# Optimization experiments

Hardware: AMD Instinct MI355X
Metric: run time of the kernel (lower is better)

The kernel has to match this reference:

```python
import jax, jax.numpy as jnp
import numpy as np

IN_DIM, OUT_DIM = 512, 512
GRID, K, NUM_STDS = 16, 2, 4
DEGREE = 3  # hardcoded in original __call__ (bspline called with 3)
NUM_CTRL = GRID + K - 1  # 17
BATCH = 4096


def bspline_basis(t, g, degree):
    """Cox-de Boor B-spline basis.
    t: (in_dim, batch) evaluation points, g: (K,) uniform knots.
    Returns basis of shape (K-1-degree, in_dim, batch)."""
    # degree-0 indicator: g[i] <= t < g[i+1]
    B = ((g[:-1, None, None] <= t[None]) & (t[None] < g[1:, None, None])).astype(t.dtype)
    for p in range(1, degree + 1):
        left = (t[None] - g[:-(p + 1), None, None]) / (g[p:-1] - g[:-(p + 1)])[:, None, None]
        right = (g[p + 1:, None, None] - t[None]) / (g[p + 1:] - g[1:-p])[:, None, None]
        B = left * B[:-1] + right * B[1:]
    return B


def setup_inputs() -> dict:
    key = jax.random.key(0)
    k1, k2, k3 = jax.random.split(key, 3)
    limit = float(np.sqrt(6.0 / (IN_DIM + OUT_DIM)))
    x = jax.random.normal(k1, (BATCH, IN_DIM), dtype=jnp.float32)
    w_b = jnp.ones((IN_DIM, OUT_DIM), dtype=jnp.float32)
    w_s = jax.random.uniform(k2, (IN_DIM, OUT_DIM), minval=-limit, maxval=limit, dtype=jnp.float32)
    control_points = jax.random.uniform(k3, (IN_DIM, OUT_DIM, NUM_CTRL), minval=-limit, maxval=limit, dtype=jnp.float32)
    grid_width = GRID / NUM_STDS
    num_aug = GRID + 1 + 2 * K
    grid_points = jnp.linspace(-K * grid_width, GRID + K * grid_width, num_aug).astype(jnp.float32)
    bound = jnp.float32(NUM_STDS * 1.0)
    return {"x": x, "w_b": w_b, "w_s": w_s, "control_points": control_points,
            "grid_points": grid_points, "bound": bound}


def reference(x, w_b, w_s, control_points, grid_points, bound):
    bound = jax.lax.stop_gradient(bound)
    g = jax.lax.stop_gradient(grid_points)
    xt = jnp.clip(x.T, -bound, bound)                      # (in_dim, batch)
    silu = xt * jax.nn.sigmoid(xt)
    bias = jnp.einsum('io,ib->ob', w_b, silu)              # (out_dim, batch)
    basis = bspline_basis(xt, g, DEGREE)                    # (nc, in_dim, batch)
    D = w_s[:, :, None] * control_points                    # (in_dim, out_dim, nc)
    spline = jnp.einsum('ioc,cib->ob', D, basis)            # single GEMM, (out_dim, batch)
    return (bias + spline).T                                # (batch, out_dim)
```

## Files before the change

### kernel.cpp

```cpp
#include <hip/hip_runtime.h>
#include <hip/hip_bf16.h>

#define IN_DIM 512
#define OUT_DIM 512
#define BATCH 4096
#define NC 9
#define KDIM (IN_DIM * NC)
#define NCTRL 17
#define TM 128
#define TN 64
#define BK 64
#define NT (KDIM / BK)
#define BUF_ELEMS 12288
#define BUF_BYTES 24576

typedef unsigned short ushort_t;
typedef __attribute__((ext_vector_type(8))) short short8;
typedef __attribute__((ext_vector_type(4))) float f32x4;

__device__ inline ushort_t to_bf16(float f) {
    union { float f; unsigned int i; } v; v.f = f;
    unsigned int r = v.i + 0x7FFF + ((v.i >> 16) & 1);
    return (ushort_t)(r >> 16);
}

__device__ inline void gld16(const ushort_t* g, void* l) {
    __builtin_amdgcn_global_load_lds(
        (const __attribute__((address_space(1))) void*)g,
        (__attribute__((address_space(3))) void*)l, 16, 0, 0);
}


__global__ void prep_A(const float* __restrict__ w_b, const float* __restrict__ w_s,
                       const float* __restrict__ ctrl, ushort_t* __restrict__ A) {
    int tid = blockIdx.x * 256 + threadIdx.x;
    int i = tid & (IN_DIM - 1);
    int o = tid >> 9;
    float ws = w_s[i * OUT_DIM + o];
    float wb = w_b[i * OUT_DIM + o];
    const float* cp = ctrl + (size_t)(i * OUT_DIM + o) * NCTRL;
    size_t rbase = (size_t)o * KDIM;
    int swz = (o & 7) << 3;
    int k0 = i * NC;
#pragma unroll
    for (int c = 0; c < 8; c++) A[rbase + ((k0 + c) ^ swz)] = to_bf16(ws * cp[c]);
    A[rbase + ((k0 + 8) ^ swz)] = to_bf16(wb);
}

__global__ __launch_bounds__(512) void prep_B(const float* __restrict__ x,
                                              const float* __restrict__ g,
                                              const float* __restrict__ bound_p,
                                              ushort_t* __restrict__ Bt) {
    __shared__ ushort_t rowbuf[KDIM];
    int b = blockIdx.x;
    int i = threadIdx.x;
    float bound = bound_p[0];
    float t = x[(size_t)b * IN_DIM + i];
    t = fminf(fmaxf(t, -bound), bound);
    float u = (t + 8.0f) * 0.625f;
    int j = (int)u;
    j = min(max(j, 2), 7);
    float gj[6];
#pragma unroll
    for (int r = 0; r < 6; r++) gj[r] = g[j - 2 + r];
    const float invph[4] = {0.f, 0.625f, 0.3125f, 0.2083333333f};
    float Nv[4]; Nv[0] = 1.0f;
    float lv[4], rv[4];
#pragma unroll
    for (int p = 1; p <= 3; p++) {
        lv[p] = t - gj[3 - p];
        rv[p] = gj[2 + p] - t;
        float saved = 0.0f;
#pragma unroll
        for (int r = 0; r < p; r++) {
            float temp = Nv[r] * invph[p];
            Nv[r] = saved + rv[r + 1] * temp;
            saved = lv[p - r] * temp;
        }
        Nv[p] = saved;
    }
    int c0 = j - 3;
    int swz = (b & 7) << 3;
    int k0 = i * NC;
#pragma unroll
    for (int c = 0; c < 8; c++) {
        float v = 0.0f;
        v = (c == c0    ) ? Nv[0] : v;
        v = (c == c0 + 1) ? Nv[1] : v;
        v = (c == c0 + 2) ? Nv[2] : v;
        v = (c == c0 + 3) ? Nv[3] : v;
        rowbuf[(k0 + c) ^ swz] = to_bf16(v);
    }
    float sg = 1.0f / (1.0f + __expf(-t));
    rowbuf[(k0 + 8) ^ swz] = to_bf16(t * sg);
    __syncthreads();
    const uint4* s = (const uint4*)rowbuf;
    uint4* d = (uint4*)(Bt + (size_t)b * KDIM);
    d[i] = s[i];
    if (i < 64) d[512 + i] = s[512 + i];
}

__global__ __launch_bounds__(512) void gemm_kan(const ushort_t* __restrict__ A,
                                                const ushort_t* __restrict__ Bt,
                                                float* __restrict__ out) {
    __shared__ ushort_t ring[4 * BUF_ELEMS];
    int tid = threadIdx.x;
    int lane = tid & 63;
    int w = tid >> 6;
    int bid = blockIdx.x;
    int ot = bid >> 5;
    int bt = bid & 31;
    int brow0 = bt * TM;
    int ocol0 = ot * TN;

    int wr = w >> 1;
    int wc = w & 1;

    f32x4 acc[2][2];
#pragma unroll
    for (int m = 0; m < 2; m++)
#pragma unroll
        for (int n = 0; n < 2; n++) acc[m][n] = (f32x4){0.f, 0.f, 0.f, 0.f};

    int lr = lane >> 3;
    int lcb = (lane & 7) * 8;
    const ushort_t* src[3];
    int ldsoff[3];
#pragma unroll
    for (int i = 0; i < 3; i++) {
        int f = w * 3 + i;
        const ushort_t* basep = (f < 16)
            ? Bt + (size_t)(brow0 + f * 8 + lr) * KDIM
            : A  + (size_t)(ocol0 + (f - 16) * 8 + lr) * KDIM;
        src[i] = basep + lcb;
        ldsoff[i] = f * 1024;
    }
    char* ringb = (char*)ring;

#define STAGE(T) do { int bb_ = ((T) & 3) * BUF_BYTES;                         \
    _Pragma("unroll") for (int i_ = 0; i_ < 3; i_++)                           \
        gld16(src[i_] + (size_t)(T) * BK, ringb + bb_ + ldsoff[i_]); } while (0)

#define COMPUTE(T) do {                                                        \
    const ushort_t* Xs_ = ring + ((T) & 3) * BUF_ELEMS;                        \
    const ushort_t* Ys_ = Xs_ + TM * BK;                                       \
    int xrow_ = wr * 32 + (lane & 15);                                         \
    int yrow_ = wc * 32 + (lane & 15);                                         \
    int swz_ = (lane & 7) << 3;                                                \
    _Pragma("unroll") for (int kk_ = 0; kk_ < 2; kk_++) {                      \
        int kofs_ = (kk_ * 32 + ((lane >> 4) << 3)) ^ swz_;                    \
        short8 xf0 = *(const short8*)&Xs_[(xrow_     ) * BK + kofs_];          \
        short8 xf1 = *(const short8*)&Xs_[(xrow_ + 16) * BK + kofs_];          \
        short8 yf0 = *(const short8*)&Ys_[(yrow_     ) * BK + kofs_];          \
        short8 yf1 = *(const short8*)&Ys_[(yrow_ + 16) * BK + kofs_];          \
        acc[0][0] = __builtin_amdgcn_mfma_f32_16x16x32_bf16(xf0, yf0, acc[0][0], 0, 0, 0); \
        acc[0][1] = __builtin_amdgcn_mfma_f32_16x16x32_bf16(xf0, yf1, acc[0][1], 0, 0, 0); \
        acc[1][0] = __builtin_amdgcn_mfma_f32_16x16x32_bf16(xf1, yf0, acc[1][0], 0, 0, 0); \
        acc[1][1] = __builtin_amdgcn_mfma_f32_16x16x32_bf16(xf1, yf1, acc[1][1], 0, 0, 0); \
    } } while (0)

#define WAITVM(N) asm volatile("s_waitcnt vmcnt(" #N ")" ::: "memory")
#define BARRIER() do { __builtin_amdgcn_sched_barrier(0);                      \
    __builtin_amdgcn_s_barrier();                                             \
    __builtin_amdgcn_sched_barrier(0);                                        \
    asm volatile("" ::: "memory"); } while (0)

    STAGE(0); STAGE(1); STAGE(2);
    for (int t = 0; t < NT - 3; ++t) {
        WAITVM(6);
        BARRIER();
        STAGE(t + 3);
        COMPUTE(t);
    }
    WAITVM(6); BARRIER(); COMPUTE(NT - 3);
    WAITVM(3); BARRIER(); COMPUTE(NT - 2);
    WAITVM(0); BARRIER(); COMPUTE(NT - 1);

    int rgrp = (lane >> 4) * 4;
    int cidx = lane & 15;
#pragma unroll
    for (int m = 0; m < 2; m++) {
#pragma unroll
        for (int n = 0; n < 2; n++) {
            int o_idx = ocol0 + wc * 32 + n * 16 + cidx;
            int b_base = brow0 + wr * 32 + m * 16 + rgrp;
#pragma unroll
            for (int r = 0; r < 4; r++)
                out[(size_t)(b_base + r) * OUT_DIM + o_idx] = acc[m][n][r];
        }
    }
#undef STAGE
#undef COMPUTE
#undef WAITVM
#undef BARRIER
}

extern "C" void kernel_launch(void* const* d_in, const int* in_sizes, int n_in,
                              void* d_out, int out_size, void* d_ws, size_t ws_size,
                              hipStream_t stream) {
    const float* x     = (const float*)d_in[0];
    const float* w_b   = (const float*)d_in[1];
    const float* w_s   = (const float*)d_in[2];
    const float* ctrl  = (const float*)d_in[3];
    const float* g     = (const float*)d_in[4];
    const float* bound = (const float*)d_in[5];
    float* out = (float*)d_out;

    ushort_t* Abuf = (ushort_t*)d_ws;
    ushort_t* Bbuf = (ushort_t*)((char*)d_ws + (size_t)(8u << 20));

    prep_A<<<IN_DIM * OUT_DIM / 256, 256, 0, stream>>>(w_b, w_s, ctrl, Abuf);
    prep_B<<<BATCH, 512, 0, stream>>>(x, g, bound, Bbuf);
    gemm_kan<<<(BATCH / TM) * (OUT_DIM / TN), 512, 0, stream>>>(Abuf, Bbuf, out);
}
```

Baseline: 52.44 us.

## Enlarge GEMM tile to 128x128 with split-K atomics and fuse prep kernels

Result: slower. 73.79 us (+40.7%).

```diff
diff --git a/kernel.cpp b/kernel.cpp
--- a/kernel.cpp
+++ b/kernel.cpp
@@ -8,11 +8,13 @@
 #define KDIM (IN_DIM * NC)
 #define NCTRL 17
 #define TM 128
-#define TN 64
+#define TN 128
 #define BK 64
-#define NT (KDIM / BK)
-#define BUF_ELEMS 12288
-#define BUF_BYTES 24576
+#define SPLITK 2
+#define KSLICE (KDIM / SPLITK)
+#define NT (KSLICE / BK)
+#define BUF_ELEMS ((TM + TN) * BK)
+#define BUF_BYTES (BUF_ELEMS * 2)
 
 typedef unsigned short ushort_t;
 typedef __attribute__((ext_vector_type(8))) short short8;
@@ -31,162 +33,168 @@
 }
 
 
-__global__ void prep_A(const float* __restrict__ w_b, const float* __restrict__ w_s,
-                       const float* __restrict__ ctrl, ushort_t* __restrict__ A) {
-    int tid = blockIdx.x * 256 + threadIdx.x;
-    int i = tid & (IN_DIM - 1);
-    int o = tid >> 9;
-    float ws = w_s[i * OUT_DIM + o];
-    float wb = w_b[i * OUT_DIM + o];
-    const float* cp = ctrl + (size_t)(i * OUT_DIM + o) * NCTRL;
-    size_t rbase = (size_t)o * KDIM;
-    int swz = (o & 7) << 3;
-    int k0 = i * NC;
-#pragma unroll
-    for (int c = 0; c < 8; c++) A[rbase + ((k0 + c) ^ swz)] = to_bf16(ws * cp[c]);
-    A[rbase + ((k0 + 8) ^ swz)] = to_bf16(wb);
-}
-
-__global__ __launch_bounds__(512) void prep_B(const float* __restrict__ x,
-                                              const float* __restrict__ g,
-                                              const float* __restrict__ bound_p,
-                                              ushort_t* __restrict__ Bt) {
+__global__ __launch_bounds__(512) void prep_AB(const float* __restrict__ x,
+                                               const float* __restrict__ g,
+                                               const float* __restrict__ bound_p,
+                                               const float* __restrict__ w_b,
+                                               const float* __restrict__ w_s,
+                                               const float* __restrict__ ctrl,
+                                               ushort_t* __restrict__ Bt,
+                                               ushort_t* __restrict__ A) {
     __shared__ ushort_t rowbuf[KDIM];
-    int b = blockIdx.x;
+    int blk = blockIdx.x;
     int i = threadIdx.x;
-    float bound = bound_p[0];
-    float t = x[(size_t)b * IN_DIM + i];
-    t = fminf(fmaxf(t, -bound), bound);
-    float u = (t + 8.0f) * 0.625f;
-    int j = (int)u;
-    j = min(max(j, 2), 7);
-    float gj[6];
-#pragma unroll
-    for (int r = 0; r < 6; r++) gj[r] = g[j - 2 + r];
-    const float invph[4] = {0.f, 0.625f, 0.3125f, 0.2083333333f};
-    float Nv[4]; Nv[0] = 1.0f;
-    float lv[4], rv[4];
-#pragma unroll
-    for (int p = 1; p <= 3; p++) {
-        lv[p] = t - gj[3 - p];
-        rv[p] = gj[2 + p] - t;
-        float saved = 0.0f;
-#pragma unroll
-        for (int r = 0; r < p; r++) {
-            float temp = Nv[r] * invph[p];
-            Nv[r] = saved + rv[r + 1] * temp;
-            saved = lv[p - r] * temp;
+    ushort_t* dstrow;
+    if (blk < BATCH) {
+        int b = blk;
+        float bound = bound_p[0];
+        float t = x[(size_t)b * IN_DIM + i];
+        t = fminf(fmaxf(t, -bound), bound);
+        float u = (t + 8.0f) * 0.625f;
+        int j = (int)u;
+        j = min(max(j, 2), 7);
+        float gj[6];
+#pragma unroll
+        for (int r = 0; r < 6; r++) gj[r] = g[j - 2 + r];
+        const float invph[4] = {0.f, 0.625f, 0.3125f, 0.2083333333f};
+        float Nv[4]; Nv[0] = 1.0f;
+        float lv[4], rv[4];
+#pragma unroll
+        for (int p = 1; p <= 3; p++) {
+            lv[p] = t - gj[3 - p];
+            rv[p] = gj[2 + p] - t;
+            float saved = 0.0f;
+#pragma unroll
+            for (int r = 0; r < p; r++) {
+                float temp = Nv[r] * invph[p];
+                Nv[r] = saved + rv[r + 1] * temp;
+                saved = lv[p - r] * temp;
+            }
+            Nv[p] = saved;
         }
-        Nv[p] = saved;
-    }
-    int c0 = j - 3;
-    int swz = (b & 7) << 3;
-    int k0 = i * NC;
-#pragma unroll
-    for (int c = 0; c < 8; c++) {
-        float v = 0.0f;
-        v = (c == c0    ) ? Nv[0] : v;
-        v = (c == c0 + 1) ? Nv[1] : v;
-        v = (c == c0 + 2) ? Nv[2] : v;
-        v = (c == c0 + 3) ? Nv[3] : v;
-        rowbuf[(k0 + c) ^ swz] = to_bf16(v);
-    }
-    float sg = 1.0f / (1.0f + __expf(-t));
-    rowbuf[(k0 + 8) ^ swz] = to_bf16(t * sg);
+        int c0 = j - 3;
+        int swz = (b & 7) << 3;
+        int k0 = i * NC;
+#pragma unroll
+        for (int c = 0; c < 8; c++) {
+            float v = 0.0f;
+            v = (c == c0    ) ? Nv[0] : v;
+            v = (c == c0 + 1) ? Nv[1] : v;
+            v = (c == c0 + 2) ? Nv[2] : v;
+            v = (c == c0 + 3) ? Nv[3] : v;
+            rowbuf[(k0 + c) ^ swz] = to_bf16(v);
+        }
+        float sg = 1.0f / (1.0f + __expf(-t));
+        rowbuf[(k0 + 8) ^ swz] = to_bf16(t * sg);
+        dstrow = Bt + (size_t)b * KDIM;
+    } else {
+        int o = blk - BATCH;
+        float ws = w_s[(size_t)i * OUT_DIM + o];
+        float wb = w_b[(size_t)i * OUT_DIM + o];
+        const float* cp = ctrl + ((size_t)i * OUT_DIM + o) * NCTRL;
+        int swz = (o & 7) << 3;
+        int k0 = i * NC;
+#pragma unroll
+        for (int c = 0; c < 8; c++) rowbuf[(k0 + c) ^ swz] = to_bf16(ws * cp[c]);
+        rowbuf[(k0 + 8) ^ swz] = to_bf16(wb);
+        dstrow = A + (size_t)o * KDIM;
+    }
     __syncthreads();
     const uint4* s = (const uint4*)rowbuf;
-    uint4* d = (uint4*)(Bt + (size_t)b * KDIM);
+    uint4* d = (uint4*)dstrow;
     d[i] = s[i];
     if (i < 64) d[512 + i] = s[512 + i];
 }
 
-__global__ __launch_bounds__(512) void gemm_kan(const ushort_t* __restrict__ A,
+__global__ __launch_bounds__(256) void gemm_kan(const ushort_t* __restrict__ A,
                                                 const ushort_t* __restrict__ Bt,
                                                 float* __restrict__ out) {
-    __shared__ ushort_t ring[4 * BUF_ELEMS];
+    extern __shared__ ushort_t ring[];
     int tid = threadIdx.x;
     int lane = tid & 63;
     int w = tid >> 6;
     int bid = blockIdx.x;
-    int ot = bid >> 5;
+    int ot = bid >> 6;
+    int kz = (bid >> 5) & 1;
     int bt = bid & 31;
     int brow0 = bt * TM;
     int ocol0 = ot * TN;
+    int k0 = kz * KSLICE;
 
     int wr = w >> 1;
     int wc = w & 1;
 
-    f32x4 acc[2][2];
-#pragma unroll
-    for (int m = 0; m < 2; m++)
-#pragma unroll
-        for (int n = 0; n < 2; n++) acc[m][n] = (f32x4){0.f, 0.f, 0.f, 0.f};
+    f32x4 acc[4][4];
+#pragma unroll
+    for (int m = 0; m < 4; m++)
+#pragma unroll
+        for (int n = 0; n < 4; n++) acc[m][n] = (f32x4){0.f, 0.f, 0.f, 0.f};
 
     int lr = lane >> 3;
     int lcb = (lane & 7) * 8;
-    const ushort_t* src[3];
-    int ldsoff[3];
-#pragma unroll
-    for (int i = 0; i < 3; i++) {
-        int f = w * 3 + i;
+    const ushort_t* src[8];
+    int ldsoff[8];
+#pragma unroll
+    for (int i = 0; i < 8; i++) {
+        int f = w * 8 + i;
         const ushort_t* basep = (f < 16)
             ? Bt + (size_t)(brow0 + f * 8 + lr) * KDIM
             : A  + (size_t)(ocol0 + (f - 16) * 8 + lr) * KDIM;
-        src[i] = basep + lcb;
+        src[i] = basep + k0 + lcb;
         ldsoff[i] = f * 1024;
     }
     char* ringb = (char*)ring;
 
 #define STAGE(T) do { int bb_ = ((T) & 3) * BUF_BYTES;                         \
-    _Pragma("unroll") for (int i_ = 0; i_ < 3; i_++)                           \
+    _Pragma("unroll") for (int i_ = 0; i_ < 8; i_++)                           \
         gld16(src[i_] + (size_t)(T) * BK, ringb + bb_ + ldsoff[i_]); } while (0)
 
 #define COMPUTE(T) do {                                                        \
     const ushort_t* Xs_ = ring + ((T) & 3) * BUF_ELEMS;                        \
     const ushort_t* Ys_ = Xs_ + TM * BK;                                       \
-    int xrow_ = wr * 32 + (lane & 15);                                         \
-    int yrow_ = wc * 32 + (lane & 15);                                         \
+    int xrow_ = wr * 64 + (lane & 15);                                         \
+    int yrow_ = wc * 64 + (lane & 15);                                         \
     int swz_ = (lane & 7) << 3;                                                \
     _Pragma("unroll") for (int kk_ = 0; kk_ < 2; kk_++) {                      \
         int kofs_ = (kk_ * 32 + ((lane >> 4) << 3)) ^ swz_;                    \
-        short8 xf0 = *(const short8*)&Xs_[(xrow_     ) * BK + kofs_];          \
-        short8 xf1 = *(const short8*)&Xs_[(xrow_ + 16) * BK + kofs_];          \
-        short8 yf0 = *(const short8*)&Ys_[(yrow_     ) * BK + kofs_];          \
-        short8 yf1 = *(const short8*)&Ys_[(yrow_ + 16) * BK + kofs_];          \
-        acc[0][0] = __builtin_amdgcn_mfma_f32_16x16x32_bf16(xf0, yf0, acc[0][0], 0, 0, 0); \
-        acc[0][1] = __builtin_amdgcn_mfma_f32_16x16x32_bf16(xf0, yf1, acc[0][1], 0, 0, 0); \
-        acc[1][0] = __builtin_amdgcn_mfma_f32_16x16x32_bf16(xf1, yf0, acc[1][0], 0, 0, 0); \
-        acc[1][1] = __builtin_amdgcn_mfma_f32_16x16x32_bf16(xf1, yf1, acc[1][1], 0, 0, 0); \
+        short8 xf[4], yf[4];                                                   \
+        _Pragma("unroll") for (int m_ = 0; m_ < 4; m_++)                       \
+            xf[m_] = *(const short8*)&Xs_[(xrow_ + m_ * 16) * BK + kofs_];     \
+        _Pragma("unroll") for (int n_ = 0; n_ < 4; n_++)                       \
+            yf[n_] = *(const short8*)&Ys_[(yrow_ + n_ * 16) * BK + kofs_];     \
+        _Pragma("unroll") for (int m_ = 0; m_ < 4; m_++)                       \
+            _Pragma("unroll") for (int n_ = 0; n_ < 4; n_++)                   \
+                acc[m_][n_] = __builtin_amdgcn_mfma_f32_16x16x32_bf16(         \
+                    xf[m_], yf[n_], acc[m_][n_], 0, 0, 0);                     \
     } } while (0)
 
 #define WAITVM(N) asm volatile("s_waitcnt vmcnt(" #N ")" ::: "memory")
 #define BARRIER() do { __builtin_amdgcn_sched_barrier(0);                      \
-    __builtin_amdgcn_s_barrier();                                             \
-    __builtin_amdgcn_sched_barrier(0);                                        \
-    asm volatile("" ::: "memory"); } while (0)
+    __builtin_amdgcn_s_barrier();                                              \
+    __builtin_amdgcn_sched_barrier(0); } while (0)
 
     STAGE(0); STAGE(1); STAGE(2);
     for (int t = 0; t < NT - 3; ++t) {
-        WAITVM(6);
+        WAITVM(16);
         BARRIER();
         STAGE(t + 3);
         COMPUTE(t);
     }
-    WAITVM(6); BARRIER(); COMPUTE(NT - 3);
-    WAITVM(3); BARRIER(); COMPUTE(NT - 2);
-    WAITVM(0); BARRIER(); COMPUTE(NT - 1);
+    WAITVM(16); BARRIER(); COMPUTE(NT - 3);
+    WAITVM(8);  BARRIER(); COMPUTE(NT - 2);
+    WAITVM(0);  BARRIER(); COMPUTE(NT - 1);
 
     int rgrp = (lane >> 4) * 4;
     int cidx = lane & 15;
 #pragma unroll
-    for (int m = 0; m < 2; m++) {
-#pragma unroll
-        for (int n = 0; n < 2; n++) {
-            int o_idx = ocol0 + wc * 32 + n * 16 + cidx;
-            int b_base = brow0 + wr * 32 + m * 16 + rgrp;
+    for (int m = 0; m < 4; m++) {
+#pragma unroll
+        for (int n = 0; n < 4; n++) {
+            int o_idx = ocol0 + wc * 64 + n * 16 + cidx;
+            int b_base = brow0 + wr * 64 + m * 16 + rgrp;
 #pragma unroll
             for (int r = 0; r < 4; r++)
-                out[(size_t)(b_base + r) * OUT_DIM + o_idx] = acc[m][n][r];
+                atomicAdd(out + (size_t)(b_base + r) * OUT_DIM + o_idx, acc[m][n][r]);
         }
     }
 #undef STAGE
@@ -209,7 +217,15 @@
     ushort_t* Abuf = (ushort_t*)d_ws;
     ushort_t* Bbuf = (ushort_t*)((char*)d_ws + (size_t)(8u << 20));
 
-    prep_A<<<IN_DIM * OUT_DIM / 256, 256, 0, stream>>>(w_b, w_s, ctrl, Abuf);
-    prep_B<<<BATCH, 512, 0, stream>>>(x, g, bound, Bbuf);
-    gemm_kan<<<(BATCH / TM) * (OUT_DIM / TN), 512, 0, stream>>>(Abuf, Bbuf, out);
-}
+    static int lds_ok = 0;
+    if (!lds_ok) {
+        hipFuncSetAttribute((const void*)gemm_kan,
+                            hipFuncAttributeMaxDynamicSharedMemorySize,
+                            4 * BUF_BYTES);
+        lds_ok = 1;
+    }
+
+    hipMemsetAsync(d_out, 0, (size_t)BATCH * OUT_DIM * sizeof(float), stream);
+    prep_AB<<<BATCH + OUT_DIM, 512, 0, stream>>>(x, g, bound, w_b, w_s, ctrl, Bbuf, Abuf);
+    gemm_kan<<<(BATCH / TM) * (OUT_DIM / TN) * SPLITK, 256, 4 * BUF_BYTES, stream>>>(Abuf, Bbuf, out);
+}
```
